# Kernel optimization log

Measured on AMD Instinct MI355X. Metric: run time of the kernel, lower is better.

The kernel has to match this reference:

```python
import jax, jax.numpy as jnp
import numpy as np

N_NODES = 4096
N_EDGES = 8192
N_GRAPHS = 256
D_NODE = 64
D_EDGE = 32
H = 256


def setup_inputs() -> dict:
    key = jax.random.key(0)
    ks = jax.random.split(key, 16)
    s = lambda d: 1.0 / np.sqrt(d)
    inp = {
        "x": jax.random.normal(ks[0], (N_NODES, D_NODE), dtype=jnp.float32),
        "edge_index": jax.random.randint(ks[1], (2, N_EDGES), 0, N_NODES),
        "edge_attr": jax.random.normal(ks[2], (N_EDGES, D_EDGE), dtype=jnp.float32),
        "batch": jnp.sort(jax.random.randint(ks[3], (N_NODES,), 0, N_GRAPHS)),
        # conv1: edge MLP 32 -> 64*256, root weight 64->256, bias 256
        "nn1_w": jax.random.normal(ks[4], (D_EDGE, D_NODE * H), dtype=jnp.float32) * s(D_EDGE),
        "nn1_b": jnp.zeros((D_NODE * H,), dtype=jnp.float32),
        "root1_w": jax.random.normal(ks[5], (D_NODE, H), dtype=jnp.float32) * s(D_NODE),
        "bias1": jnp.zeros((H,), dtype=jnp.float32),
        # conv2: edge MLP 32 -> 256*256, root weight 256->256, bias 256
        "nn2_w": jax.random.normal(ks[6], (D_EDGE, H * H), dtype=jnp.float32) * s(D_EDGE),
        "nn2_b": jnp.zeros((H * H,), dtype=jnp.float32),
        "root2_w": jax.random.normal(ks[7], (H, H), dtype=jnp.float32) * s(H),
        "bias2": jnp.zeros((H,), dtype=jnp.float32),
        # readout MLP: 256 -> 128 -> 1
        "lin1_w": jax.random.normal(ks[8], (H, H // 2), dtype=jnp.float32) * s(H),
        "lin1_b": jnp.zeros((H // 2,), dtype=jnp.float32),
        "lin2_w": jax.random.normal(ks[9], (H // 2, 1), dtype=jnp.float32) * s(H // 2),
        "lin2_b": jnp.zeros((1,), dtype=jnp.float32),
    }
    return inp


def nnconv(x, src, dst, edge_attr, nn_w, nn_b, root_w, bias, out_c):
    # PyG NNConv (aggr='add'): per-edge weight matrix from edge MLP,
    # message = x[src] @ W_e, scatter-add at dst, plus root transform + bias.
    e = edge_attr.shape[0]
    in_c = x.shape[1]
    w_e = (edge_attr @ nn_w + nn_b).reshape(e, in_c, out_c)  # [E, in, out]
    msg = jnp.einsum('ei,eio->eo', x[src], w_e)              # [E, out]
    agg = jax.ops.segment_sum(msg, dst, num_segments=x.shape[0])
    return agg + x @ root_w + bias


def reference(x, edge_index, edge_attr, batch,
              nn1_w, nn1_b, root1_w, bias1,
              nn2_w, nn2_b, root2_w, bias2,
              lin1_w, lin1_b, lin2_w, lin2_b):
    src, dst = edge_index[0], edge_index[1]
    h = nnconv(x, src, dst, edge_attr, nn1_w, nn1_b, root1_w, bias1, H)
    h = jax.nn.relu(h)
    h = nnconv(h, src, dst, edge_attr, nn2_w, nn2_b, root2_w, bias2, H)
    # global mean pool over graphs
    sums = jax.ops.segment_sum(h, batch, num_segments=N_GRAPHS)
    cnts = jax.ops.segment_sum(jnp.ones((h.shape[0],), h.dtype), batch, num_segments=N_GRAPHS)
    pooled = sums / jnp.maximum(cnts, 1.0)[:, None]
    # dropout is identity in eval mode
    z = jax.nn.relu(pooled @ lin1_w + lin1_b)
    return jax.nn.sigmoid(z @ lin2_w + lin2_b)  # [N_GRAPHS, 1]
```

## Files before the change

kernel.cpp:

```cpp
#include <hip/hip_runtime.h>
#include <math.h>

#define N_NODES 4096
#define N_EDGES 8192
#define N_GRAPHS 256
#define D_NODE 64
#define D_EDGE 32
#define HH 256

#define K1 2176
#define K2 8704
#define NSL1 8
#define NSL2 12

typedef _Float16 half8v __attribute__((ext_vector_type(8)));
typedef _Float16 half4v __attribute__((ext_vector_type(4)));
typedef float floatx4 __attribute__((ext_vector_type(4)));

static const size_t OFF_S    = 0;
static const size_t OFF_BT1  = 17825792;
static const size_t OFF_BT2  = 18104320;
static const size_t OFF_CP   = 19218432;
static const size_t OFF_H    = 25509888;
static const size_t OFF_INT  = 26034176;

__device__ void csr_body(const int* __restrict__ dst,
                         int* __restrict__ starts,
                         int* __restrict__ elist) {
    __shared__ int cnt[4096];
    __shared__ int ps[256];
    int t = threadIdx.x;
#pragma unroll
    for (int i = 0; i < 16; ++i) cnt[t * 16 + i] = 0;
    __syncthreads();
#pragma unroll
    for (int i = 0; i < 32; ++i) atomicAdd(&cnt[dst[i * 256 + t]], 1);
    __syncthreads();
    int v[16]; int s = 0;
#pragma unroll
    for (int i = 0; i < 16; ++i) { v[i] = cnt[t * 16 + i]; s += v[i]; }
    ps[t] = s;
    __syncthreads();
    for (int off = 1; off < 256; off <<= 1) {
        int tv = (t >= off) ? ps[t - off] : 0;
        __syncthreads();
        ps[t] += tv;
        __syncthreads();
    }
    int excl = ps[t] - s;
#pragma unroll
    for (int i = 0; i < 16; ++i) {
        starts[t * 16 + i] = excl;
        cnt[t * 16 + i] = excl;
        excl += v[i];
    }
    if (t == 255) starts[4096] = excl;
    __syncthreads();
#pragma unroll
    for (int i = 0; i < 32; ++i) {
        int e = i * 256 + t;
        int d = dst[e];
        int p = atomicAdd(&cnt[d], 1);
        elist[p] = e;
    }
}

__device__ void packT_body(const float* __restrict__ w,
                           const float* __restrict__ b,
                           const float* __restrict__ rw,
                           _Float16* __restrict__ BT,
                           int kk0, int o0, int K,
                           int wlim, int blim, int wshift, int wmask, int wrow) {
    __shared__ float T[64][65];
    int t = threadIdx.x;
    int ol = t & 63, kb = t >> 6;
#pragma unroll
    for (int p = 0; p < 16; ++p) {
        int kl = p * 4 + kb;
        int kk = kk0 + kl, o = o0 + ol;
        float v;
        if (kk < wlim)      v = w[(kk >> wshift) * wrow + (kk & wmask) * 256 + o];
        else if (kk < blim) v = b[(kk - wlim) * 256 + o];
        else                v = rw[(kk - blim) * 256 + o];
        T[kl][ol] = v;
    }
    __syncthreads();
    int kl2 = t & 63, ob = t >> 6;
#pragma unroll
    for (int p = 0; p < 16; ++p) {
        int ol2 = p * 4 + ob;
        BT[(size_t)(o0 + ol2) * K + kk0 + kl2] = (_Float16)T[kl2][ol2];
    }
}

__global__ __launch_bounds__(256) void prep_k(const int* __restrict__ dst,
                                              int* __restrict__ starts,
                                              int* __restrict__ elist,
                                              const float* __restrict__ w1,
                                              const float* __restrict__ b1,
                                              const float* __restrict__ r1,
                                              const float* __restrict__ w2,
                                              const float* __restrict__ b2,
                                              const float* __restrict__ r2,
                                              _Float16* __restrict__ BT1,
                                              _Float16* __restrict__ BT2) {
    int bx = blockIdx.x, by = blockIdx.y;
    if (bx == 0) {
        if (by == 0) csr_body(dst, starts, elist);
        return;
    }
    int pbx = bx - 1, o0 = by * 64;
    if (pbx < K1 / 64)
        packT_body(w1, b1, r1, BT1, pbx * 64, o0, K1, 2048, 2112, 6, 63, 16384);
    else
        packT_body(w2, b2, r2, BT2, (pbx - K1 / 64) * 64, o0, K2, 8192, 8448, 8, 255, 65536);
}

__global__ __launch_bounds__(64) void s1_k(const float* __restrict__ x,
                                           const float* __restrict__ ea,
                                           const int* __restrict__ src,
                                           const int* __restrict__ starts,
                                           const int* __restrict__ elist,
                                           _Float16* __restrict__ S) {
    int n = blockIdx.x, t = threadIdx.x;
    int cg = t & 7, kg = t >> 3;
    int i0 = cg * 8;
    float acc[5][8] = {};
    int e0 = starts[n], e1 = starts[n + 1];
    for (int ie = e0; ie < e1; ++ie) {
        int e = elist[ie];
        int sn = src[e];
        float4 f0 = *(const float4*)&x[sn * 64 + i0];
        float4 f1 = *(const float4*)&x[sn * 64 + i0 + 4];
        float xv[8] = {f0.x, f0.y, f0.z, f0.w, f1.x, f1.y, f1.z, f1.w};
#pragma unroll
        for (int j = 0; j < 4; ++j) {
            float va = ea[e * 32 + kg + 8 * j];
#pragma unroll
            for (int c = 0; c < 8; ++c) acc[j][c] += va * xv[c];
        }
        if (kg == 0) {
#pragma unroll
            for (int c = 0; c < 8; ++c) acc[4][c] += xv[c];
        }
    }
    _Float16* row = S + (size_t)n * K1;
#pragma unroll
    for (int j = 0; j < 4; ++j) {
        int k = kg + 8 * j;
        half8v o;
#pragma unroll
        for (int c = 0; c < 8; ++c) o[c] = (_Float16)acc[j][c];
        *(half8v*)&row[k * 64 + i0] = o;
    }
    if (kg == 0) {
        half8v o;
#pragma unroll
        for (int c = 0; c < 8; ++c) o[c] = (_Float16)acc[4][c];
        *(half8v*)&row[32 * 64 + i0] = o;
    }
    if (kg == 1) {
        float4 f0 = *(const float4*)&x[n * 64 + i0];
        float4 f1 = *(const float4*)&x[n * 64 + i0 + 4];
        half8v o;
        o[0] = (_Float16)f0.x; o[1] = (_Float16)f0.y; o[2] = (_Float16)f0.z; o[3] = (_Float16)f0.w;
        o[4] = (_Float16)f1.x; o[5] = (_Float16)f1.y; o[6] = (_Float16)f1.z; o[7] = (_Float16)f1.w;
        *(half8v*)&row[2112 + i0] = o;
    }
}

__global__ __launch_bounds__(256) void s2_k(const _Float16* __restrict__ h,
                                            const float* __restrict__ ea,
                                            const int* __restrict__ src,
                                            const int* __restrict__ starts,
                                            const int* __restrict__ elist,
                                            _Float16* __restrict__ S) {
    int n = blockIdx.x, t = threadIdx.x;
    int cg = t & 31, kg = t >> 5;
    int i0 = cg * 8;
    float acc[5][8] = {};
    int e0 = starts[n], e1 = starts[n + 1];
    for (int ie = e0; ie < e1; ++ie) {
        int e = elist[ie];
        int sn = src[e];
        half8v hv = *(const half8v*)&h[sn * 256 + i0];
        float xv[8];
#pragma unroll
        for (int c = 0; c < 8; ++c) xv[c] = (float)hv[c];
#pragma unroll
        for (int j = 0; j < 4; ++j) {
            float va = ea[e * 32 + kg + 8 * j];
#pragma unroll
            for (int c = 0; c < 8; ++c) acc[j][c] += va * xv[c];
        }
        if (kg == 0) {
#pragma unroll
            for (int c = 0; c < 8; ++c) acc[4][c] += xv[c];
        }
    }
    _Float16* row = S + (size_t)n * K2;
#pragma unroll
    for (int j = 0; j < 4; ++j) {
        int k = kg + 8 * j;
        half8v o;
#pragma unroll
        for (int c = 0; c < 8; ++c) o[c] = (_Float16)acc[j][c];
        *(half8v*)&row[k * 256 + i0] = o;
    }
    if (kg == 0) {
        half8v o;
#pragma unroll
        for (int c = 0; c < 8; ++c) o[c] = (_Float16)acc[4][c];
        *(half8v*)&row[32 * 256 + i0] = o;
    }
    if (kg == 1) {
        half8v hv = *(const half8v*)&h[n * 256 + i0];
        *(half8v*)&row[8448 + i0] = hv;
    }
}

__device__ __forceinline__ void async_copy16(const void* g, void* l) {
    __builtin_amdgcn_global_load_lds(
        (__attribute__((address_space(1))) unsigned int*)(g),
        (__attribute__((address_space(3))) unsigned int*)(l), 16, 0, 0);
}

__global__ __launch_bounds__(256, 3) void gemm_f16(const _Float16* __restrict__ A,
                                                   const _Float16* __restrict__ BT,
                                                   _Float16* __restrict__ Cpart,
                                                   int K, int NC, int Z) {
    __shared__ _Float16 lds[17408];
    _Float16* As = lds;
    _Float16* Bs = lds + 128 * 64;
    int tid = threadIdx.x;
    int w = tid >> 6, l = tid & 63;
    int mt = blockIdx.y, nt = blockIdx.x, z = blockIdx.z;
    int c0 = z * NC / Z, c1 = (z + 1) * NC / Z;
    int k0 = c0 * 64;
    int wm = w & 1, wn = w >> 1;

    int lr = l >> 3, lc = l & 7;
    int gc = lc ^ lr;
    const _Float16* gA0 = A  + (size_t)(mt * 128 + w * 32 + lr) * K + k0 + gc * 8;
    const _Float16* gB0 = BT + (size_t)(nt * 128 + w * 32 + lr) * K + k0 + gc * 8;

    int lm = l & 15, q4 = l >> 4;
    int sw = lm & 7;

    floatx4 acc[4][4] = {};

    for (int s = c0; s < c1; ++s) {
#pragma unroll
        for (int q = 0; q < 4; ++q) {
            async_copy16(gA0 + (size_t)q * 8 * K, As + (w * 32 + q * 8) * 64);
            async_copy16(gB0 + (size_t)q * 8 * K, Bs + (w * 32 + q * 8) * 64);
        }
        gA0 += 64; gB0 += 64;
        __syncthreads();
#pragma unroll
        for (int kw = 0; kw < 2; ++kw) {
            int ck = ((kw * 4 + q4) ^ sw) * 8;
            half8v af[4], bf[4];
#pragma unroll
            for (int i = 0; i < 4; ++i)
                af[i] = *(const half8v*)&As[(wm * 64 + i * 16 + lm) * 64 + ck];
#pragma unroll
            for (int j = 0; j < 4; ++j)
                bf[j] = *(const half8v*)&Bs[(wn * 64 + j * 16 + lm) * 64 + ck];
#pragma unroll
            for (int i = 0; i < 4; ++i)
#pragma unroll
                for (int j = 0; j < 4; ++j)
                    acc[i][j] = __builtin_amdgcn_mfma_f32_16x16x32_f16(af[i], bf[j], acc[i][j], 0, 0, 0);
        }
        __syncthreads();
    }

    _Float16* ep = lds + w * 4352;
#pragma unroll
    for (int i = 0; i < 4; ++i)
#pragma unroll
        for (int j = 0; j < 4; ++j)
#pragma unroll
            for (int r = 0; r < 4; ++r)
                ep[(i * 16 + q4 * 4 + r) * 68 + j * 16 + lm] = (_Float16)acc[i][j][r];
    __syncthreads();
    _Float16* Cp = Cpart + (size_t)z * (N_NODES * HH);
    int row8 = l >> 3, colg = (l & 7) * 8;
    int gm0 = mt * 128 + wm * 64, gn0 = nt * 128 + wn * 64;
#pragma unroll
    for (int i8 = 0; i8 < 8; ++i8) {
        int rr = i8 * 8 + row8;
        half4v lo = *(const half4v*)&ep[rr * 68 + colg];
        half4v hi = *(const half4v*)&ep[rr * 68 + colg + 4];
        half8v v;
        v[0] = lo[0]; v[1] = lo[1]; v[2] = lo[2]; v[3] = lo[3];
        v[4] = hi[0]; v[5] = hi[1]; v[6] = hi[2]; v[7] = hi[3];
        *(half8v*)&Cp[(size_t)(gm0 + rr) * HH + gn0 + colg] = v;
    }
}

__global__ __launch_bounds__(256) void hep_k(const _Float16* __restrict__ Cp,
                                             const float* __restrict__ bias,
                                             _Float16* __restrict__ h) {
    int idx = (blockIdx.x * 256 + threadIdx.x) * 8;
    float a[8] = {};
#pragma unroll
    for (int zz = 0; zz < NSL1; ++zz) {
        half8v v = *(const half8v*)(Cp + (size_t)zz * (N_NODES * HH) + idx);
#pragma unroll
        for (int j = 0; j < 8; ++j) a[j] += (float)v[j];
    }
    int col = idx & 255;
    half8v o;
#pragma unroll
    for (int j = 0; j < 8; ++j) o[j] = (_Float16)fmaxf(a[j] + bias[col + j], 0.f);
    *(half8v*)(h + idx) = o;
}

__global__ __launch_bounds__(256) void poolread_k(const _Float16* __restrict__ Cp,
                                                  const int* __restrict__ batch,
                                                  const float* __restrict__ bias2,
                                                  const float* __restrict__ l1w,
                                                  const float* __restrict__ l1b,
                                                  const float* __restrict__ l2w,
                                                  const float* __restrict__ l2b,
                                                  float* __restrict__ out) {
    int g = blockIdx.x, t = threadIdx.x;
    __shared__ int bnds[2];
    __shared__ float sp[256];
    __shared__ float sz[128];
    if (t < 2) {
        int target = g + t;
        int lo = 0, hi = N_NODES;
        while (lo < hi) { int mid = (lo + hi) >> 1; if (batch[mid] < target) lo = mid + 1; else hi = mid; }
        bnds[t] = lo;
    }
    __syncthreads();
    int lo = bnds[0], hi = bnds[1];
    float s = 0.f;
    for (int n = lo; n < hi; ++n) {
#pragma unroll
        for (int zz = 0; zz < NSL2; ++zz)
            s += (float)Cp[(size_t)zz * (N_NODES * HH) + (size_t)n * HH + t];
    }
    sp[t] = (hi > lo) ? (s / (float)(hi - lo) + bias2[t]) : 0.f;
    __syncthreads();
    if (t < 128) {
        float a = l1b[t];
#pragma unroll 8
        for (int i = 0; i < 256; ++i) a += sp[i] * l1w[i * 128 + t];
        sz[t] = fmaxf(a, 0.f) * l2w[t];
    }
    __syncthreads();
    for (int ss = 64; ss > 0; ss >>= 1) {
        if (t < ss) sz[t] += sz[t + ss];
        __syncthreads();
    }
    if (t == 0) {
        float zz = sz[0] + l2b[0];
        out[g] = 1.0f / (1.0f + expf(-zz));
    }
}

extern "C" void kernel_launch(void* const* d_in, const int* in_sizes, int n_in,
                              void* d_out, int out_size, void* d_ws, size_t ws_size,
                              hipStream_t stream) {
    const float* x       = (const float*)d_in[0];
    const int*   ei      = (const int*)d_in[1];
    const float* ea      = (const float*)d_in[2];
    const int*   batch   = (const int*)d_in[3];
    const float* nn1_w   = (const float*)d_in[4];
    const float* nn1_b   = (const float*)d_in[5];
    const float* root1_w = (const float*)d_in[6];
    const float* bias1   = (const float*)d_in[7];
    const float* nn2_w   = (const float*)d_in[8];
    const float* nn2_b   = (const float*)d_in[9];
    const float* root2_w = (const float*)d_in[10];
    const float* bias2   = (const float*)d_in[11];
    const float* lin1_w  = (const float*)d_in[12];
    const float* lin1_b  = (const float*)d_in[13];
    const float* lin2_w  = (const float*)d_in[14];
    const float* lin2_b  = (const float*)d_in[15];
    float* out = (float*)d_out;
    float* ws  = (float*)d_ws;

    _Float16* S   = (_Float16*)(ws + OFF_S);
    _Float16* BT1 = (_Float16*)(ws + OFF_BT1);
    _Float16* BT2 = (_Float16*)(ws + OFF_BT2);
    _Float16* Cp  = (_Float16*)(ws + OFF_CP);
    _Float16* h   = (_Float16*)(ws + OFF_H);
    int* ip     = (int*)(ws + OFF_INT);
    int* starts = ip;
    int* elist  = ip + 4100;

    const int* srcv = ei;
    const int* dstv = ei + N_EDGES;

    prep_k<<<dim3(1 + K1 / 64 + K2 / 64, 4), 256, 0, stream>>>(
        dstv, starts, elist, nn1_w, nn1_b, root1_w, nn2_w, nn2_b, root2_w, BT1, BT2);

    s1_k<<<4096, 64, 0, stream>>>(x, ea, srcv, starts, elist, S);

    gemm_f16<<<dim3(2, 32, NSL1), 256, 0, stream>>>(S, BT1, Cp, K1, K1 / 64, NSL1);

    hep_k<<<512, 256, 0, stream>>>(Cp, bias1, h);

    s2_k<<<4096, 256, 0, stream>>>(h, ea, srcv, starts, elist, S);

    gemm_f16<<<dim3(2, 32, NSL2), 256, 0, stream>>>(S, BT2, Cp, K2, K2 / 64, NSL2);

    poolread_k<<<N_GRAPHS, 256, 0, stream>>>(Cp, batch, bias2,
                                             lin1_w, lin1_b, lin2_w, lin2_b, out);
}
```

Measured before the change: 199.7 us.

## Fuse split-K reduction into GEMM via last-block tile counters

Each split-K GEMM block atomically increments a per-tile counter after writing its partial, and the last block for a tile sums all Z partials, adds the bias (plus ReLU for layer 1), and writes the final activations. This removes the separate hep_k launch and the 12-way partial reduction inside poolread_k, so pooling now reads a single fp32 h2 buffer. The cost is a serialized tail: one block per tile does the whole reduction with 64 float accumulators per thread, which risks register spills under launch_bounds(256,3) and adds threadfence/atomic overhead.

```diff
diff --git a/kernel.cpp b/kernel.cpp
--- a/kernel.cpp
+++ b/kernel.cpp
@@ -22,7 +22,8 @@
 static const size_t OFF_BT2  = 18104320;
 static const size_t OFF_CP   = 19218432;
 static const size_t OFF_H    = 25509888;
-static const size_t OFF_INT  = 26034176;
+static const size_t OFF_H2   = 26034176;
+static const size_t OFF_INT  = 27082752;
 
 __device__ void csr_body(const int* __restrict__ dst,
                          int* __restrict__ starts,
@@ -96,6 +97,7 @@
 __global__ __launch_bounds__(256) void prep_k(const int* __restrict__ dst,
                                               int* __restrict__ starts,
                                               int* __restrict__ elist,
+                                              int* __restrict__ tilecnt,
                                               const float* __restrict__ w1,
                                               const float* __restrict__ b1,
                                               const float* __restrict__ r1,
@@ -107,6 +109,7 @@
     int bx = blockIdx.x, by = blockIdx.y;
     if (bx == 0) {
         if (by == 0) csr_body(dst, starts, elist);
+        else if (by == 1 && threadIdx.x < 128) tilecnt[threadIdx.x] = 0;
         return;
     }
     int pbx = bx - 1, o0 = by * 64;
@@ -228,7 +231,12 @@
 __global__ __launch_bounds__(256, 3) void gemm_f16(const _Float16* __restrict__ A,
                                                    const _Float16* __restrict__ BT,
                                                    _Float16* __restrict__ Cpart,
-                                                   int K, int NC, int Z) {
+                                                   int K, int NC, int Z,
+                                                   const float* __restrict__ bias,
+                                                   _Float16* __restrict__ out16,
+                                                   float* __restrict__ out32,
+                                                   int relu,
+                                                   int* __restrict__ tilecnt) {
     __shared__ _Float16 lds[17408];
     _Float16* As = lds;
     _Float16* Bs = lds + 128 * 64;
@@ -298,29 +306,58 @@
         v[4] = hi[0]; v[5] = hi[1]; v[6] = hi[2]; v[7] = hi[3];
         *(half8v*)&Cp[(size_t)(gm0 + rr) * HH + gn0 + colg] = v;
     }
-}
-
-__global__ __launch_bounds__(256) void hep_k(const _Float16* __restrict__ Cp,
-                                             const float* __restrict__ bias,
-                                             _Float16* __restrict__ h) {
-    int idx = (blockIdx.x * 256 + threadIdx.x) * 8;
-    float a[8] = {};
-#pragma unroll
-    for (int zz = 0; zz < NSL1; ++zz) {
-        half8v v = *(const half8v*)(Cp + (size_t)zz * (N_NODES * HH) + idx);
-#pragma unroll
-        for (int j = 0; j < 8; ++j) a[j] += (float)v[j];
-    }
-    int col = idx & 255;
-    half8v o;
-#pragma unroll
-    for (int j = 0; j < 8; ++j) o[j] = (_Float16)fmaxf(a[j] + bias[col + j], 0.f);
-    *(half8v*)(h + idx) = o;
-}
-
-__global__ __launch_bounds__(256) void poolread_k(const _Float16* __restrict__ Cp,
+
+    __syncthreads();
+    __shared__ int isLast;
+    if (tid == 0) {
+        __threadfence();
+        int old = atomicAdd(&tilecnt[mt * 2 + nt], 1);
+        isLast = (old == Z - 1);
+    }
+    __syncthreads();
+    if (!isLast) return;
+    __threadfence();
+
+    int r = tid >> 1, ch = (tid & 1) * 64;
+    int grow = mt * 128 + r;
+    int gcol = nt * 128 + ch;
+    float facc[64] = {};
+    for (int zz = 0; zz < Z; ++zz) {
+        const _Float16* p = Cpart + (size_t)zz * (N_NODES * HH) + (size_t)grow * HH + gcol;
+#pragma unroll
+        for (int q = 0; q < 8; ++q) {
+            half8v v = *(const half8v*)(p + q * 8);
+#pragma unroll
+            for (int j = 0; j < 8; ++j) facc[q * 8 + j] += (float)v[j];
+        }
+    }
+    if (out16) {
+#pragma unroll
+        for (int q = 0; q < 8; ++q) {
+            half8v o;
+#pragma unroll
+            for (int j = 0; j < 8; ++j) {
+                float v = facc[q * 8 + j] + bias[gcol + q * 8 + j];
+                if (relu) v = fmaxf(v, 0.f);
+                o[j] = (_Float16)v;
+            }
+            *(half8v*)&out16[(size_t)grow * HH + gcol + q * 8] = o;
+        }
+    } else {
+#pragma unroll
+        for (int q = 0; q < 16; ++q) {
+            float4 o;
+            o.x = facc[q * 4 + 0] + bias[gcol + q * 4 + 0];
+            o.y = facc[q * 4 + 1] + bias[gcol + q * 4 + 1];
+            o.z = facc[q * 4 + 2] + bias[gcol + q * 4 + 2];
+            o.w = facc[q * 4 + 3] + bias[gcol + q * 4 + 3];
+            *(float4*)&out32[(size_t)grow * HH + gcol + q * 4] = o;
+        }
+    }
+}
+
+__global__ __launch_bounds__(256) void poolread_k(const float* __restrict__ h2,
                                                   const int* __restrict__ batch,
-                                                  const float* __restrict__ bias2,
                                                   const float* __restrict__ l1w,
                                                   const float* __restrict__ l1b,
                                                   const float* __restrict__ l2w,
@@ -339,12 +376,8 @@
     __syncthreads();
     int lo = bnds[0], hi = bnds[1];
     float s = 0.f;
-    for (int n = lo; n < hi; ++n) {
-#pragma unroll
-        for (int zz = 0; zz < NSL2; ++zz)
-            s += (float)Cp[(size_t)zz * (N_NODES * HH) + (size_t)n * HH + t];
-    }
-    sp[t] = (hi > lo) ? (s / (float)(hi - lo) + bias2[t]) : 0.f;
+    for (int n = lo; n < hi; ++n) s += h2[(size_t)n * HH + t];
+    sp[t] = (hi > lo) ? (s / (float)(hi - lo)) : 0.f;
     __syncthreads();
     if (t < 128) {
         float a = l1b[t];
@@ -390,26 +423,29 @@
     _Float16* BT2 = (_Float16*)(ws + OFF_BT2);
     _Float16* Cp  = (_Float16*)(ws + OFF_CP);
     _Float16* h   = (_Float16*)(ws + OFF_H);
-    int* ip     = (int*)(ws + OFF_INT);
-    int* starts = ip;
-    int* elist  = ip + 4100;
+    float*    h2  = ws + OFF_H2;
+    int* ip      = (int*)(ws + OFF_INT);
+    int* starts  = ip;
+    int* elist   = ip + 4100;
+    int* tilecnt = ip + 12300;
 
     const int* srcv = ei;
     const int* dstv = ei + N_EDGES;
 
     prep_k<<<dim3(1 + K1 / 64 + K2 / 64, 4), 256, 0, stream>>>(
-        dstv, starts, elist, nn1_w, nn1_b, root1_w, nn2_w, nn2_b, root2_w, BT1, BT2);
+        dstv, starts, elist, tilecnt,
+        nn1_w, nn1_b, root1_w, nn2_w, nn2_b, root2_w, BT1, BT2);
 
     s1_k<<<4096, 64, 0, stream>>>(x, ea, srcv, starts, elist, S);
 
-    gemm_f16<<<dim3(2, 32, NSL1), 256, 0, stream>>>(S, BT1, Cp, K1, K1 / 64, NSL1);
-
-    hep_k<<<512, 256, 0, stream>>>(Cp, bias1, h);
+    gemm_f16<<<dim3(2, 32, NSL1), 256, 0, stream>>>(S, BT1, Cp, K1, K1 / 64, NSL1,
+                                                    bias1, h, nullptr, 1, tilecnt);
 
     s2_k<<<4096, 256, 0, stream>>>(h, ea, srcv, starts, elist, S);
 
-    gemm_f16<<<dim3(2, 32, NSL2), 256, 0, stream>>>(S, BT2, Cp, K2, K2 / 64, NSL2);
-
-    poolread_k<<<N_GRAPHS, 256, 0, stream>>>(Cp, batch, bias2,
+    gemm_f16<<<dim3(2, 32, NSL2), 256, 0, stream>>>(S, BT2, Cp, K2, K2 / 64, NSL2,
+                                                    bias2, nullptr, h2, 0, tilecnt + 64);
+
+    poolread_k<<<N_GRAPHS, 256, 0, stream>>>(h2, batch,
                                              lin1_w, lin1_b, lin2_w, lin2_b, out);
 }
```

New measurement: 269.0 us. 34.7% more time.
